# Kernel optimization log

Hardware: AMD Instinct MI355X
Metric: run time of the kernel (lower is better)

Reference implementation:

```python
import jax, jax.numpy as jnp
import numpy as np

N = 50000        # total nodes across batch
K = 16           # max neighbors per node (padded with index 0)
E = 800000       # directed edges / messages
B = 1024         # molecules
MAXM = 48        # max nodes per molecule (padded with index 0)
FEATURE_FDIM = 9
ALL_FDIM = 10    # feature_dist_graph (9) + reshaped rij distance (1)
H = 64           # hidden_dim
NUM_ITERS = 2
NEG_INF = -1e9


def setup_inputs() -> dict:
    key = jax.random.key(0)
    ks = jax.random.split(key, 16)
    s = 1.0 / np.sqrt(H)
    return {
        "target_features": jax.random.normal(ks[0], (N, FEATURE_FDIM), jnp.float32),
        "feature_dist_graph": jax.random.normal(ks[1], (E, ALL_FDIM - 1), jnp.float32),
        "rij_dist_pairs": jax.random.uniform(ks[2], (E,), jnp.float32),
        "start_end_env": jax.random.randint(ks[3], (N, K), 0, N + 1),
        "b_scope": jax.random.randint(ks[4], (N, K), 0, E),
        "l_scope": jax.random.randint(ks[5], (B, MAXM), 0, N + 1),
        "scope_update": jax.random.randint(ks[6], (E,), 0, N + 1),
        "scope_update_lig": jax.random.randint(ks[7], (E,), 0, N + 1),
        "W_emb": jax.random.uniform(ks[8], (FEATURE_FDIM, H), jnp.float32, 0.1, 0.9),
        "b_emb": jnp.zeros((H,), jnp.float32),
        "W_dist": jax.random.uniform(ks[9], (ALL_FDIM, H), jnp.float32, 0.1, 0.9),
        "b_dist": jnp.zeros((H,), jnp.float32),
        "W_gat": jax.random.normal(ks[10], (H, H), jnp.float32) * s,
        "Wm_gat": jax.random.normal(ks[11], (H, H), jnp.float32) * s,
        "a_gat": jax.random.normal(ks[12], (2 * H,), jnp.float32) * s,
    }


def reference(target_features, feature_dist_graph, rij_dist_pairs,
              start_end_env, b_scope, l_scope, scope_update, scope_update_lig,
              W_emb, b_emb, W_dist, b_dist, W_gat, Wm_gat, a_gat):
    # node embedding over origin features
    h = target_features @ W_emb + b_emb                        # [N, H]
    # edge message embedding over pair features + distance
    msg_in = jnp.concatenate([feature_dist_graph, rij_dist_pairs[:, None]], axis=1)
    message = msg_in @ W_dist + b_dist                         # [E, H]
    # prepend zero pad row (index 0 = padding for ragged gathers)
    hp = jnp.concatenate([jnp.zeros((1, H), h.dtype), h], axis=0)  # [N+1, H]
    pad_mask = (start_end_env == 0)                            # [N, K]
    upd_mask = (scope_update_lig > 0).astype(h.dtype)[:, None]  # [E, 1]
    for _ in range(NUM_ITERS):
        nb = hp[start_end_env]                                 # [N, K, H] gather neighbors
        mg = message[b_scope]                                  # [N, K, H] gather messages
        Wn = nb @ W_gat                                        # [N, K, H]
        Wm = mg @ Wm_gat                                       # [N, K, H]
        # GAT attention logits: leaky_relu(a^T [Wn || Wm])
        logits = jax.nn.leaky_relu(
            jnp.einsum('nkh,h->nk', Wn, a_gat[:H]) +
            jnp.einsum('nkh,h->nk', Wm, a_gat[H:]), 0.2)       # [N, K]
        logits = jnp.where(pad_mask, NEG_INF, logits)
        alpha = jax.nn.softmax(logits, axis=1)                 # [N, K]
        new_h = jax.nn.elu(jnp.einsum('nk,nkh->nh', alpha, Wn + Wm))  # [N, H]
        hp = jnp.concatenate([jnp.zeros((1, H), new_h.dtype), new_h], axis=0)
        # scatter updated node features back into edge messages
        message = hp[scope_update] * upd_mask                  # [E, H]
    cmp_enc = hp[l_scope]                                      # [B, MAXM, H]
    return cmp_enc.sum(axis=1)                                 # [B, H]
```

## Files before the change

kernel.cpp:

```cpp
#include <hip/hip_runtime.h>
#include <hip/hip_bf16.h>

#define N_NODES 50000
#define K_NB 16
#define E_EDGES 800000
#define B_MOL 1024
#define MAXM_M 48
#define FDIM 9
#define ADIM 10
#define H 64
#define NEG_INF_F (-1e9f)
#define PRE_NODE_BLOCKS 196
#define EDGE_BLOCKS 3125

typedef __bf16 bf16x8 __attribute__((ext_vector_type(8)));
typedef float f32x4 __attribute__((ext_vector_type(4)));

__device__ inline float readlane_f(float v, int l) {
    return __int_as_float(__builtin_amdgcn_readlane(__float_as_int(v), l));
}
__device__ inline int readlane_i(int v, int l) {
    return __builtin_amdgcn_readlane(v, l);
}
__device__ inline float bf2f(unsigned u) {
    return __uint_as_float(u << 16);
}
__device__ inline unsigned short f2bf(float f) {
    unsigned x = __float_as_uint(f);
    return (unsigned short)((x + 0x7fffu + ((x >> 16) & 1u)) >> 16);
}

#define GLOAD_U16(dst, voff, sbase) \
    asm volatile("global_load_ushort %0, %1, %2" : "=v"(dst) : "v"(voff), "s"(sbase))
#define GLOAD_F32(dst, voff, sbase) \
    asm volatile("global_load_dword %0, %1, %2" : "=v"(dst) : "v"(voff), "s"(sbase))

#define DRAIN16(a) \
    asm volatile("s_waitcnt vmcnt(0)" \
        : "+v"(a[0]), "+v"(a[1]), "+v"(a[2]), "+v"(a[3]), \
          "+v"(a[4]), "+v"(a[5]), "+v"(a[6]), "+v"(a[7]), \
          "+v"(a[8]), "+v"(a[9]), "+v"(a[10]), "+v"(a[11]), \
          "+v"(a[12]), "+v"(a[13]), "+v"(a[14]), "+v"(a[15]))
#define HOLD16(a) \
    asm volatile("" \
        : "+v"(a[0]), "+v"(a[1]), "+v"(a[2]), "+v"(a[3]), \
          "+v"(a[4]), "+v"(a[5]), "+v"(a[6]), "+v"(a[7]), \
          "+v"(a[8]), "+v"(a[9]), "+v"(a[10]), "+v"(a[11]), \
          "+v"(a[12]), "+v"(a[13]), "+v"(a[14]), "+v"(a[15]))

__global__ __launch_bounds__(256) void k_fold(
    const float* __restrict__ W_emb, const float* __restrict__ b_emb,
    const float* __restrict__ W_dist, const float* __restrict__ b_dist,
    const float* __restrict__ W_gat, const float* __restrict__ Wm_gat,
    const float* __restrict__ a_gat,
    float* __restrict__ W2, float* __restrict__ c2,
    float* __restrict__ W3, float* __restrict__ c3,
    float* __restrict__ wa, float* __restrict__ ca,
    float* __restrict__ va, float* __restrict__ vb,
    float* __restrict__ wv9, float* __restrict__ cv,
    unsigned short* __restrict__ WintT)
{
    __shared__ float s_va[64], s_vb[64];
    int tid = threadIdx.x;
    int h = tid & 63, g = tid >> 6;
    if (g == 0) {
        float acc = 0.f;
        for (int t = 0; t < H; ++t) acc += W_gat[h * H + t] * a_gat[t];
        s_va[h] = acc; va[h] = acc;
    } else if (g == 1) {
        float acc = 0.f;
        for (int t = 0; t < H; ++t) acc += Wm_gat[h * H + t] * a_gat[H + t];
        s_vb[h] = acc; vb[h] = acc;
    } else if (g == 2) {
        float acc = 0.f;
        for (int t = 0; t < H; ++t) acc += b_dist[t] * Wm_gat[t * H + h];
        c2[h] = acc;
    } else {
        float acc = 0.f;
        for (int t = 0; t < H; ++t) acc += b_emb[t] * W_gat[t * H + h];
        c3[h] = acc;
    }
    __syncthreads();
    for (int q = tid; q < 640; q += 256) {
        int j = q >> 6, hh = q & 63;
        float acc = 0.f;
        for (int t = 0; t < H; ++t) acc += W_dist[j * H + t] * Wm_gat[t * H + hh];
        W2[q] = acc;
    }
    for (int q = tid; q < 576; q += 256) {
        int j = q >> 6, hh = q & 63;
        float acc = 0.f;
        for (int t = 0; t < H; ++t) acc += W_emb[j * H + t] * W_gat[t * H + hh];
        W3[q] = acc;
    }
    for (int q = tid; q < H * 2 * H; q += 256) {
        int n = q >> 7, k = q & 127;
        float v = (k & 1) ? Wm_gat[(k >> 1) * H + n] : W_gat[(k >> 1) * H + n];
        WintT[q] = f2bf(v);
    }
    if (tid < ADIM) {
        float acc = 0.f;
        for (int t = 0; t < H; ++t) acc += W_dist[tid * H + t] * s_vb[t];
        wa[tid] = acc;
    } else if (tid == ADIM) {
        float acc = 0.f;
        for (int t = 0; t < H; ++t) acc += b_dist[t] * s_vb[t];
        ca[0] = acc;
    } else if (tid >= 16 && tid < 16 + FDIM) {
        int j = tid - 16;
        float acc = 0.f;
        for (int t = 0; t < H; ++t) acc += W_emb[j * H + t] * s_va[t];
        wv9[j] = acc;
    } else if (tid == 31) {
        float acc = 0.f;
        for (int t = 0; t < H; ++t) acc += b_emb[t] * s_va[t];
        cv[0] = acc;
    }
}

__global__ __launch_bounds__(256) void k_pre(
    const float* __restrict__ tf, const float* __restrict__ fdg,
    const float* __restrict__ rij,
    const int* __restrict__ su, const int* __restrict__ sul,
    const float* __restrict__ wa, const float* __restrict__ ca,
    const float* __restrict__ wv9, const float* __restrict__ cv,
    float* __restrict__ t1A, unsigned short* __restrict__ tfp,
    unsigned short* __restrict__ emsg, int* __restrict__ sue)
{
    int bid = blockIdx.x;
    if (bid < PRE_NODE_BLOCKS) {
        int n = bid * 256 + threadIdx.x;
        if (n == 0) {
            t1A[0] = 0.f;
            uint4 z = make_uint4(0, 0, 0, 0);
            ((uint4*)tfp)[0] = z; ((uint4*)tfp)[1] = z;
        }
        if (n >= N_NODES) return;
        float f[FDIM];
        float acc = cv[0];
#pragma unroll
        for (int j = 0; j < FDIM; ++j) {
            f[j] = tf[n * FDIM + j];
            acc += f[j] * wv9[j];
        }
        t1A[n + 1] = acc;
        unsigned rec[8];
#pragma unroll
        for (int j = 0; j < 4; ++j)
            rec[j] = (unsigned)f2bf(f[2 * j]) | ((unsigned)f2bf(f[2 * j + 1]) << 16);
        rec[4] = (unsigned)f2bf(f[8]);
        rec[5] = 0; rec[6] = 0; rec[7] = 0;
        uint4* dst = (uint4*)(tfp + (size_t)(n + 1) * 16);
        dst[0] = make_uint4(rec[0], rec[1], rec[2], rec[3]);
        dst[1] = make_uint4(rec[4], rec[5], rec[6], rec[7]);
    } else {
        int e = (bid - PRE_NODE_BLOCKS) * 256 + threadIdx.x;
        float f[ADIM];
#pragma unroll
        for (int j = 0; j < FDIM; ++j) f[j] = fdg[(size_t)e * FDIM + j];
        f[FDIM] = rij[e];
        float acc = ca[0];
#pragma unroll
        for (int j = 0; j < ADIM; ++j) acc += f[j] * wa[j];
        unsigned rec[8];
#pragma unroll
        for (int j = 0; j < 5; ++j)
            rec[j] = (unsigned)f2bf(f[2 * j]) | ((unsigned)f2bf(f[2 * j + 1]) << 16);
        rec[5] = __float_as_uint(acc);
        rec[6] = 0; rec[7] = 0;
        uint4* dst = (uint4*)(emsg + (size_t)e * 16);
        dst[0] = make_uint4(rec[0], rec[1], rec[2], rec[3]);
        dst[1] = make_uint4(rec[4], rec[5], rec[6], rec[7]);
        sue[e] = (sul[e] > 0) ? su[e] : 0;
    }
}

__global__ __launch_bounds__(256) void k_gat1(
    const int* __restrict__ sse, const int* __restrict__ bsc,
    const float* __restrict__ t1A, const unsigned short* __restrict__ tfp,
    const unsigned short* __restrict__ emsg,
    const float* __restrict__ W2, const float* __restrict__ c2,
    const float* __restrict__ W3, const float* __restrict__ c3,
    const float* __restrict__ va, const float* __restrict__ vb,
    unsigned short* __restrict__ hp2bf, float* __restrict__ t1B,
    float* __restrict__ t2B)
{
    int wave = threadIdx.x >> 6;
    int lane = threadIdx.x & 63;
    int n = blockIdx.x * 4 + wave;
    if (n == 0) {
        hp2bf[lane] = 0;
        if (lane == 0) { t1B[0] = 0.f; t2B[0] = 0.f; }
    }
    if (n >= N_NODES) return;

    int kidx = 0, ke = 0;
    float lg = NEG_INF_F;
    if (lane < K_NB) {
        kidx = sse[n * K_NB + lane];
        ke   = bsc[n * K_NB + lane];
        float g2 = __uint_as_float(*(const unsigned*)(emsg + (size_t)ke * 16 + 10));
        float p = t1A[kidx] + g2;
        p = (p > 0.f) ? p : 0.2f * p;
        lg = (kidx == 0) ? NEG_INF_F : p;
    }

    unsigned wn_u[K_NB], wm_u[K_NB];
    int offr = (lane & 15) * 2;
#pragma unroll
    for (int k = 0; k < K_NB; ++k) {
        const unsigned short* pk = tfp + (size_t)readlane_i(kidx, k) * 16;
        GLOAD_U16(wn_u[k], offr, pk);
    }
#pragma unroll
    for (int k = 0; k < K_NB; ++k) {
        const unsigned short* pe = emsg + (size_t)readlane_i(ke, k) * 16;
        GLOAD_U16(wm_u[k], offr, pe);
    }

    float m = lg;
#pragma unroll
    for (int o = 8; o > 0; o >>= 1) m = fmaxf(m, __shfl_xor(m, o, 64));
    float ex = __expf(lg - m);
    float s = ex;
#pragma unroll
    for (int o = 8; o > 0; o >>= 1) s += __shfl_xor(s, o, 64);
    float alpha = ex / s;

    DRAIN16(wn_u);
    HOLD16(wm_u);

    float fr = 0.f, frm = 0.f, beta = 0.f;
#pragma unroll
    for (int k = 0; k < K_NB; ++k) {
        float ak = readlane_f(alpha, k);
        fr  += ak * bf2f(wn_u[k]);
        frm += ak * bf2f(wm_u[k]);
        beta += (readlane_i(kidx, k) > 0) ? ak : 0.f;
    }
    float acc = c2[lane] + beta * c3[lane];
#pragma unroll
    for (int j = 0; j < FDIM; ++j) acc += readlane_f(fr, j) * W3[j * H + lane];
#pragma unroll
    for (int j = 0; j < ADIM; ++j) acc += readlane_f(frm, j) * W2[j * H + lane];
    float o = (acc > 0.f) ? acc : expm1f(acc);
    hp2bf[(size_t)(n + 1) * H + lane] = f2bf(o);
    float ta = o * va[lane], tb = o * vb[lane];
#pragma unroll
    for (int q = 32; q > 0; q >>= 1) {
        ta += __shfl_xor(ta, q, 64);
        tb += __shfl_xor(tb, q, 64);
    }
    if (lane == 0) { t1B[n + 1] = ta; t2B[n + 1] = tb; }
}

__global__ __launch_bounds__(1024) void k_gat2(
    const int* __restrict__ sse, const int* __restrict__ bsc,
    const int* __restrict__ sue,
    const float* __restrict__ t1B, const float* __restrict__ t2B,
    const unsigned short* __restrict__ hp2bf,
    const unsigned short* __restrict__ WintT,
    float* __restrict__ hp3)
{
    __shared__ unsigned s_rows[16][72];
    int wave = threadIdx.x >> 6;
    int lane = threadIdx.x & 63;
    int row  = blockIdx.x * 16 + wave;
    int n    = row - 1;

    float gn = 0.f, gm = 0.f;
    if (n >= 0 && n < N_NODES) {
        int kidx = 0, ksu = 0;
        float lg = NEG_INF_F;
        if (lane < K_NB) {
            kidx = sse[n * K_NB + lane];
            int ke = bsc[n * K_NB + lane];
            ksu = sue[ke];
            float p = t1B[kidx] + t2B[ksu];
            p = (p > 0.f) ? p : 0.2f * p;
            lg = (kidx == 0) ? NEG_INF_F : p;
        }

        unsigned wn_u[K_NB], wm_u[K_NB];
        int off = lane * 2;
#pragma unroll
        for (int k = 0; k < K_NB; ++k) {
            const unsigned short* pk = hp2bf + (size_t)readlane_i(kidx, k) * H;
            GLOAD_U16(wn_u[k], off, pk);
        }
#pragma unroll
        for (int k = 0; k < K_NB; ++k) {
            const unsigned short* ps = hp2bf + (size_t)readlane_i(ksu, k) * H;
            GLOAD_U16(wm_u[k], off, ps);
        }

        float m = lg;
#pragma unroll
        for (int o = 8; o > 0; o >>= 1) m = fmaxf(m, __shfl_xor(m, o, 64));
        float ex = __expf(lg - m);
        float s = ex;
#pragma unroll
        for (int o = 8; o > 0; o >>= 1) s += __shfl_xor(s, o, 64);
        float alpha = ex / s;

        DRAIN16(wn_u);
        HOLD16(wm_u);

#pragma unroll
        for (int k = 0; k < K_NB; ++k) {
            float ak = readlane_f(alpha, k);
            gn += ak * bf2f(wn_u[k]);
            gm += ak * bf2f(wm_u[k]);
        }
    }
    s_rows[wave][lane] = (unsigned)f2bf(gn) | ((unsigned)f2bf(gm) << 16);
    __syncthreads();

    if (wave < 4) {
        int t = wave;
        int m = lane & 15, q = lane >> 4;
        union UB { uint4 u; bf16x8 v; };
        bf16x8 bfr[4];
        const unsigned short* bp = WintT + (size_t)(t * 16 + m) * 128 + q * 8;
#pragma unroll
        for (int kk = 0; kk < 4; ++kk) {
            UB ub; ub.u = *(const uint4*)(bp + kk * 32);
            bfr[kk] = ub.v;
        }
        f32x4 acc = (f32x4){0.f, 0.f, 0.f, 0.f};
#pragma unroll
        for (int kk = 0; kk < 4; ++kk) {
            UB ua; ua.u = *(const uint4*)&s_rows[m][kk * 16 + q * 4];
            acc = __builtin_amdgcn_mfma_f32_16x16x32_bf16(ua.v, bfr[kk], acc, 0, 0, 0);
        }
        int row0 = blockIdx.x * 16;
#pragma unroll
        for (int r = 0; r < 4; ++r) {
            int rr = row0 + q * 4 + r;
            if (rr <= N_NODES) {
                float v = acc[r];
                hp3[(size_t)rr * H + t * 16 + m] = (v > 0.f) ? v : expm1f(v);
            }
        }
    }
}

__global__ __launch_bounds__(256) void k_out(
    const int* __restrict__ l_scope, const float* __restrict__ hp,
    float* __restrict__ out)
{
    int wave = threadIdx.x >> 6;
    int lane = threadIdx.x & 63;
    int b = blockIdx.x * 4 + wave;
    if (b >= B_MOL) return;
    int idx48 = (lane < MAXM_M) ? l_scope[b * MAXM_M + lane] : 0;
    float v[MAXM_M];
    int off = lane * 4;
#pragma unroll
    for (int m = 0; m < MAXM_M; ++m) {
        const float* pm = hp + (size_t)readlane_i(idx48, m) * H;
        GLOAD_F32(v[m], off, pm);
    }
    asm volatile("s_waitcnt vmcnt(0)"
        : "+v"(v[0]), "+v"(v[1]), "+v"(v[2]), "+v"(v[3]),
          "+v"(v[4]), "+v"(v[5]), "+v"(v[6]), "+v"(v[7]),
          "+v"(v[8]), "+v"(v[9]), "+v"(v[10]), "+v"(v[11]),
          "+v"(v[12]), "+v"(v[13]), "+v"(v[14]), "+v"(v[15]));
    asm volatile(""
        : "+v"(v[16]), "+v"(v[17]), "+v"(v[18]), "+v"(v[19]),
          "+v"(v[20]), "+v"(v[21]), "+v"(v[22]), "+v"(v[23]),
          "+v"(v[24]), "+v"(v[25]), "+v"(v[26]), "+v"(v[27]),
          "+v"(v[28]), "+v"(v[29]), "+v"(v[30]), "+v"(v[31]));
    asm volatile(""
        : "+v"(v[32]), "+v"(v[33]), "+v"(v[34]), "+v"(v[35]),
          "+v"(v[36]), "+v"(v[37]), "+v"(v[38]), "+v"(v[39]),
          "+v"(v[40]), "+v"(v[41]), "+v"(v[42]), "+v"(v[43]),
          "+v"(v[44]), "+v"(v[45]), "+v"(v[46]), "+v"(v[47]));
    float acc = 0.f;
#pragma unroll
    for (int m = 0; m < MAXM_M; ++m) acc += v[m];
    out[b * H + lane] = acc;
}

extern "C" void kernel_launch(void* const* d_in, const int* in_sizes, int n_in,
                              void* d_out, int out_size, void* d_ws, size_t ws_size,
                              hipStream_t stream)
{
    const float* tf     = (const float*)d_in[0];
    const float* fdg    = (const float*)d_in[1];
    const float* rij    = (const float*)d_in[2];
    const int*   sse    = (const int*)d_in[3];
    const int*   bsc    = (const int*)d_in[4];
    const int*   lsc    = (const int*)d_in[5];
    const int*   su     = (const int*)d_in[6];
    const int*   sul    = (const int*)d_in[7];
    const float* W_emb  = (const float*)d_in[8];
    const float* b_emb  = (const float*)d_in[9];
    const float* W_dist = (const float*)d_in[10];
    const float* b_dist = (const float*)d_in[11];
    const float* W_gat  = (const float*)d_in[12];
    const float* Wm_gat = (const float*)d_in[13];
    const float* a_gat  = (const float*)d_in[14];
    float* out = (float*)d_out;

    char* base = (char*)d_ws;
    size_t off = 0;
    auto alloc = [&](size_t bytes) {
        char* p = base + off;
        off = (off + bytes + 255) & ~(size_t)255;
        return p;
    };
    float* W2   = (float*)alloc(640 * 4);
    float* c2   = (float*)alloc(64 * 4);
    float* W3   = (float*)alloc(640 * 4);
    float* c3   = (float*)alloc(64 * 4);
    float* wa   = (float*)alloc(16 * 4);
    float* ca   = (float*)alloc(16 * 4);
    float* va   = (float*)alloc(64 * 4);
    float* vb   = (float*)alloc(64 * 4);
    float* wv9  = (float*)alloc(16 * 4);
    float* cv   = (float*)alloc(16 * 4);
    unsigned short* WintT = (unsigned short*)alloc(64 * 128 * 2);
    float* t1A  = (float*)alloc((size_t)(N_NODES + 1) * 4);
    float* t1B  = (float*)alloc((size_t)(N_NODES + 1) * 4);
    float* t2B  = (float*)alloc((size_t)(N_NODES + 1) * 4);
    int*   sue  = (int*)alloc((size_t)E_EDGES * 4);
    unsigned short* tfp   = (unsigned short*)alloc((size_t)(N_NODES + 1) * 16 * 2);
    unsigned short* hp2bf = (unsigned short*)alloc((size_t)(N_NODES + 1) * H * 2);
    char* big = alloc((size_t)E_EDGES * 32);
    unsigned short* emsg = (unsigned short*)big;
    float* hp3 = (float*)big;

    k_fold<<<dim3(1), dim3(256), 0, stream>>>(
        W_emb, b_emb, W_dist, b_dist, W_gat, Wm_gat, a_gat,
        W2, c2, W3, c3, wa, ca, va, vb, wv9, cv, WintT);

    k_pre<<<dim3(PRE_NODE_BLOCKS + EDGE_BLOCKS), dim3(256), 0, stream>>>(
        tf, fdg, rij, su, sul, wa, ca, wv9, cv, t1A, tfp, emsg, sue);

    k_gat1<<<dim3((N_NODES + 3) / 4), dim3(256), 0, stream>>>(
        sse, bsc, t1A, tfp, emsg, W2, c2, W3, c3, va, vb, hp2bf, t1B, t2B);

    k_gat2<<<dim3((N_NODES + 16) / 16), dim3(1024), 0, stream>>>(
        sse, bsc, sue, t1B, t2B, hp2bf, WintT, hp3);

    k_out<<<dim3(B_MOL / 4), dim3(256), 0, stream>>>(lsc, hp3, out);
}
```

Measured before the change: 209.1 us.

## Gather neighbor rows with 16-byte loads and reduce across lanes in k_gat2

Replaces the 32 per-lane 2-byte gathers per node with four dwordx4 loads per lane. Each group of 8 lanes fetches one full 128-byte neighbor row, and the alpha-weighted partial sums are then reduced across row groups with xor shuffles. The feature-row loads are issued before the attention logit and softmax computation so that the memory latency overlaps with it. This cuts the number of memory instructions, at the cost of 48 extra cross-lane shuffles for the reduction. It also adds a launch-bounds occupancy hint, which may force register limits.

```diff
diff --git a/kernel.cpp b/kernel.cpp
--- a/kernel.cpp
+++ b/kernel.cpp
@@ -15,6 +15,7 @@
 
 typedef __bf16 bf16x8 __attribute__((ext_vector_type(8)));
 typedef float f32x4 __attribute__((ext_vector_type(4)));
+typedef unsigned u32x4 __attribute__((ext_vector_type(4)));
 
 __device__ inline float readlane_f(float v, int l) {
     return __int_as_float(__builtin_amdgcn_readlane(__float_as_int(v), l));
@@ -34,6 +35,8 @@
     asm volatile("global_load_ushort %0, %1, %2" : "=v"(dst) : "v"(voff), "s"(sbase))
 #define GLOAD_F32(dst, voff, sbase) \
     asm volatile("global_load_dword %0, %1, %2" : "=v"(dst) : "v"(voff), "s"(sbase))
+#define GLOAD_X4(dst, addr) \
+    asm volatile("global_load_dwordx4 %0, %1, off" : "=v"(dst) : "v"(addr))
 
 #define DRAIN16(a) \
     asm volatile("s_waitcnt vmcnt(0)" \
@@ -47,6 +50,8 @@
           "+v"(a[4]), "+v"(a[5]), "+v"(a[6]), "+v"(a[7]), \
           "+v"(a[8]), "+v"(a[9]), "+v"(a[10]), "+v"(a[11]), \
           "+v"(a[12]), "+v"(a[13]), "+v"(a[14]), "+v"(a[15]))
+#define DRAIN4X4(a, b, c, d) \
+    asm volatile("s_waitcnt vmcnt(0)" : "+v"(a), "+v"(b), "+v"(c), "+v"(d))
 
 __global__ __launch_bounds__(256) void k_fold(
     const float* __restrict__ W_emb, const float* __restrict__ b_emb,
@@ -254,7 +259,7 @@
     if (lane == 0) { t1B[n + 1] = ta; t2B[n + 1] = tb; }
 }
 
-__global__ __launch_bounds__(1024) void k_gat2(
+__global__ __launch_bounds__(1024, 8) void k_gat2(
     const int* __restrict__ sse, const int* __restrict__ bsc,
     const int* __restrict__ sue,
     const float* __restrict__ t1B, const float* __restrict__ t2B,
@@ -268,7 +273,10 @@
     int row  = blockIdx.x * 16 + wave;
     int n    = row - 1;
 
-    float gn = 0.f, gm = 0.f;
+    float accn[8], accm[8];
+#pragma unroll
+    for (int q = 0; q < 8; ++q) { accn[q] = 0.f; accm[q] = 0.f; }
+
     if (n >= 0 && n < N_NODES) {
         int kidx = 0, ksu = 0;
         float lg = NEG_INF_F;
@@ -276,24 +284,30 @@
             kidx = sse[n * K_NB + lane];
             int ke = bsc[n * K_NB + lane];
             ksu = sue[ke];
-            float p = t1B[kidx] + t2B[ksu];
-            p = (p > 0.f) ? p : 0.2f * p;
-            lg = (kidx == 0) ? NEG_INF_F : p;
-        }
-
-        unsigned wn_u[K_NB], wm_u[K_NB];
-        int off = lane * 2;
-#pragma unroll
-        for (int k = 0; k < K_NB; ++k) {
-            const unsigned short* pk = hp2bf + (size_t)readlane_i(kidx, k) * H;
-            GLOAD_U16(wn_u[k], off, pk);
-        }
-#pragma unroll
-        for (int k = 0; k < K_NB; ++k) {
-            const unsigned short* ps = hp2bf + (size_t)readlane_i(ksu, k) * H;
-            GLOAD_U16(wm_u[k], off, ps);
-        }
-
+        }
+
+        int r = lane >> 3;
+        int p = lane & 7;
+        int kn0 = __shfl(kidx, r, 64);
+        int kn1 = __shfl(kidx, r + 8, 64);
+        int km0 = __shfl(ksu,  r, 64);
+        int km1 = __shfl(ksu,  r + 8, 64);
+
+        u32x4 vn0, vn1, vm0, vm1;
+        const uint4* a0 = (const uint4*)(hp2bf + (size_t)kn0 * H) + p;
+        const uint4* a1 = (const uint4*)(hp2bf + (size_t)kn1 * H) + p;
+        const uint4* a2 = (const uint4*)(hp2bf + (size_t)km0 * H) + p;
+        const uint4* a3 = (const uint4*)(hp2bf + (size_t)km1 * H) + p;
+        GLOAD_X4(vn0, a0);
+        GLOAD_X4(vn1, a1);
+        GLOAD_X4(vm0, a2);
+        GLOAD_X4(vm1, a3);
+
+        if (lane < K_NB) {
+            float pg = t1B[kidx] + t2B[ksu];
+            pg = (pg > 0.f) ? pg : 0.2f * pg;
+            lg = (kidx == 0) ? NEG_INF_F : pg;
+        }
         float m = lg;
 #pragma unroll
         for (int o = 8; o > 0; o >>= 1) m = fmaxf(m, __shfl_xor(m, o, 64));
@@ -303,17 +317,38 @@
         for (int o = 8; o > 0; o >>= 1) s += __shfl_xor(s, o, 64);
         float alpha = ex / s;
 
-        DRAIN16(wn_u);
-        HOLD16(wm_u);
-
-#pragma unroll
-        for (int k = 0; k < K_NB; ++k) {
-            float ak = readlane_f(alpha, k);
-            gn += ak * bf2f(wn_u[k]);
-            gm += ak * bf2f(wm_u[k]);
-        }
-    }
-    s_rows[wave][lane] = (unsigned)f2bf(gn) | ((unsigned)f2bf(gm) << 16);
+        float a_r0 = __shfl(alpha, r, 64);
+        float a_r1 = __shfl(alpha, r + 8, 64);
+
+        DRAIN4X4(vn0, vn1, vm0, vm1);
+
+#pragma unroll
+        for (int q = 0; q < 4; ++q) {
+            unsigned w0 = vn0[q], w1 = vn1[q], w2 = vm0[q], w3 = vm1[q];
+            accn[2 * q]     += a_r0 * bf2f(w0 & 0xffffu) + a_r1 * bf2f(w1 & 0xffffu);
+            accn[2 * q + 1] += a_r0 * bf2f(w0 >> 16)     + a_r1 * bf2f(w1 >> 16);
+            accm[2 * q]     += a_r0 * bf2f(w2 & 0xffffu) + a_r1 * bf2f(w3 & 0xffffu);
+            accm[2 * q + 1] += a_r0 * bf2f(w2 >> 16)     + a_r1 * bf2f(w3 >> 16);
+        }
+#pragma unroll
+        for (int o = 8; o <= 32; o <<= 1) {
+#pragma unroll
+            for (int q = 0; q < 8; ++q) {
+                accn[q] += __shfl_xor(accn[q], o, 64);
+                accm[q] += __shfl_xor(accm[q], o, 64);
+            }
+        }
+    }
+
+    if (lane < 8) {
+        unsigned outp[8];
+#pragma unroll
+        for (int q = 0; q < 8; ++q)
+            outp[q] = (unsigned)f2bf(accn[q]) | ((unsigned)f2bf(accm[q]) << 16);
+        uint4* d = (uint4*)&s_rows[wave][lane * 8];
+        d[0] = make_uint4(outp[0], outp[1], outp[2], outp[3]);
+        d[1] = make_uint4(outp[4], outp[5], outp[6], outp[7]);
+    }
     __syncthreads();
 
     if (wave < 4) {
```

New measurement: 216.0 us. 3.3% more time.

## Split gat2 gathers into two row-range phases and precompose ksu index lookup

Applied to the files above, without the earlier changes.

k_gat2 now runs twice as many blocks, each phase gathering only neighbor/message rows within half of the node range, so each phase's working set of hp2bf is smaller and more cache-resident. Each phase writes a partial pre-activation into an interleaved buffer, and k_out sums the two partials and applies ELU. A new k_ksu kernel precomposes su/sul through b_scope into a per-(n,k) index array, removing a dependent indirect load from gat2. The cost is doubled attention/softmax/MFMA work in gat2, an extra kernel launch, twice the hp3 write traffic, and extra branching in the gather loops.

```diff
diff --git a/kernel.cpp b/kernel.cpp
--- a/kernel.cpp
+++ b/kernel.cpp
@@ -12,9 +12,12 @@
 #define NEG_INF_F (-1e9f)
 #define PRE_NODE_BLOCKS 196
 #define EDGE_BLOCKS 3125
+#define GAT2_NB 3126
+#define ROW_SPLIT 25000
 
 typedef __bf16 bf16x8 __attribute__((ext_vector_type(8)));
 typedef float f32x4 __attribute__((ext_vector_type(4)));
+typedef float f32x2 __attribute__((ext_vector_type(2)));
 
 __device__ inline float readlane_f(float v, int l) {
     return __int_as_float(__builtin_amdgcn_readlane(__float_as_int(v), l));
@@ -32,8 +35,8 @@
 
 #define GLOAD_U16(dst, voff, sbase) \
     asm volatile("global_load_ushort %0, %1, %2" : "=v"(dst) : "v"(voff), "s"(sbase))
-#define GLOAD_F32(dst, voff, sbase) \
-    asm volatile("global_load_dword %0, %1, %2" : "=v"(dst) : "v"(voff), "s"(sbase))
+#define GLOAD_F32X2(dst, voff, sbase) \
+    asm volatile("global_load_dwordx2 %0, %1, %2" : "=v"(dst) : "v"(voff), "s"(sbase))
 
 #define DRAIN16(a) \
     asm volatile("s_waitcnt vmcnt(0)" \
@@ -47,6 +50,12 @@
           "+v"(a[4]), "+v"(a[5]), "+v"(a[6]), "+v"(a[7]), \
           "+v"(a[8]), "+v"(a[9]), "+v"(a[10]), "+v"(a[11]), \
           "+v"(a[12]), "+v"(a[13]), "+v"(a[14]), "+v"(a[15]))
+#define HOLD16R(a, base) \
+    asm volatile("" \
+        : "+v"(a[base + 0]), "+v"(a[base + 1]), "+v"(a[base + 2]), "+v"(a[base + 3]), \
+          "+v"(a[base + 4]), "+v"(a[base + 5]), "+v"(a[base + 6]), "+v"(a[base + 7]), \
+          "+v"(a[base + 8]), "+v"(a[base + 9]), "+v"(a[base + 10]), "+v"(a[base + 11]), \
+          "+v"(a[base + 12]), "+v"(a[base + 13]), "+v"(a[base + 14]), "+v"(a[base + 15]))
 
 __global__ __launch_bounds__(256) void k_fold(
     const float* __restrict__ W_emb, const float* __restrict__ b_emb,
@@ -121,11 +130,10 @@
 __global__ __launch_bounds__(256) void k_pre(
     const float* __restrict__ tf, const float* __restrict__ fdg,
     const float* __restrict__ rij,
-    const int* __restrict__ su, const int* __restrict__ sul,
     const float* __restrict__ wa, const float* __restrict__ ca,
     const float* __restrict__ wv9, const float* __restrict__ cv,
     float* __restrict__ t1A, unsigned short* __restrict__ tfp,
-    unsigned short* __restrict__ emsg, int* __restrict__ sue)
+    unsigned short* __restrict__ emsg)
 {
     int bid = blockIdx.x;
     if (bid < PRE_NODE_BLOCKS) {
@@ -171,8 +179,16 @@
         uint4* dst = (uint4*)(emsg + (size_t)e * 16);
         dst[0] = make_uint4(rec[0], rec[1], rec[2], rec[3]);
         dst[1] = make_uint4(rec[4], rec[5], rec[6], rec[7]);
-        sue[e] = (sul[e] > 0) ? su[e] : 0;
-    }
+    }
+}
+
+__global__ __launch_bounds__(256) void k_ksu(
+    const int* __restrict__ bsc, const int* __restrict__ su,
+    const int* __restrict__ sul, int* __restrict__ ksu_nk)
+{
+    int i = blockIdx.x * 256 + threadIdx.x;
+    int e = bsc[i];
+    ksu_nk[i] = (sul[e] > 0) ? su[e] : 0;
 }
 
 __global__ __launch_bounds__(256) void k_gat1(
@@ -255,17 +271,21 @@
 }
 
 __global__ __launch_bounds__(1024) void k_gat2(
-    const int* __restrict__ sse, const int* __restrict__ bsc,
-    const int* __restrict__ sue,
+    const int* __restrict__ sse, const int* __restrict__ ksu_nk,
     const float* __restrict__ t1B, const float* __restrict__ t2B,
     const unsigned short* __restrict__ hp2bf,
     const unsigned short* __restrict__ WintT,
-    float* __restrict__ hp3)
+    float* __restrict__ hp3pp)
 {
     __shared__ unsigned s_rows[16][72];
+    int bid  = blockIdx.x;
+    int phase = (bid >= GAT2_NB) ? 1 : 0;
+    int nb   = bid - phase * GAT2_NB;
+    int lo   = phase ? ROW_SPLIT : 0;
+    int hi   = phase ? (N_NODES + 1) : ROW_SPLIT;
     int wave = threadIdx.x >> 6;
     int lane = threadIdx.x & 63;
-    int row  = blockIdx.x * 16 + wave;
+    int row  = nb * 16 + wave;
     int n    = row - 1;
 
     float gn = 0.f, gm = 0.f;
@@ -274,8 +294,7 @@
         float lg = NEG_INF_F;
         if (lane < K_NB) {
             kidx = sse[n * K_NB + lane];
-            int ke = bsc[n * K_NB + lane];
-            ksu = sue[ke];
+            ksu  = ksu_nk[n * K_NB + lane];
             float p = t1B[kidx] + t2B[ksu];
             p = (p > 0.f) ? p : 0.2f * p;
             lg = (kidx == 0) ? NEG_INF_F : p;
@@ -285,13 +304,21 @@
         int off = lane * 2;
 #pragma unroll
         for (int k = 0; k < K_NB; ++k) {
-            const unsigned short* pk = hp2bf + (size_t)readlane_i(kidx, k) * H;
-            GLOAD_U16(wn_u[k], off, pk);
+            wn_u[k] = 0u;
+            int rk = readlane_i(kidx, k);
+            if (rk >= lo && rk < hi) {
+                const unsigned short* pk = hp2bf + (size_t)rk * H;
+                GLOAD_U16(wn_u[k], off, pk);
+            }
         }
 #pragma unroll
         for (int k = 0; k < K_NB; ++k) {
-            const unsigned short* ps = hp2bf + (size_t)readlane_i(ksu, k) * H;
-            GLOAD_U16(wm_u[k], off, ps);
+            wm_u[k] = 0u;
+            int rs = readlane_i(ksu, k);
+            if (rs >= lo && rs < hi) {
+                const unsigned short* ps = hp2bf + (size_t)rs * H;
+                GLOAD_U16(wm_u[k], off, ps);
+            }
         }
 
         float m = lg;
@@ -333,20 +360,18 @@
             UB ua; ua.u = *(const uint4*)&s_rows[m][kk * 16 + q * 4];
             acc = __builtin_amdgcn_mfma_f32_16x16x32_bf16(ua.v, bfr[kk], acc, 0, 0, 0);
         }
-        int row0 = blockIdx.x * 16;
+        int row0 = nb * 16;
 #pragma unroll
         for (int r = 0; r < 4; ++r) {
             int rr = row0 + q * 4 + r;
-            if (rr <= N_NODES) {
-                float v = acc[r];
-                hp3[(size_t)rr * H + t * 16 + m] = (v > 0.f) ? v : expm1f(v);
-            }
+            if (rr >= 1 && rr <= N_NODES)
+                hp3pp[((size_t)(rr - 1) * H + t * 16 + m) * 2 + phase] = acc[r];
         }
     }
 }
 
 __global__ __launch_bounds__(256) void k_out(
-    const int* __restrict__ l_scope, const float* __restrict__ hp,
+    const int* __restrict__ l_scope, const float* __restrict__ hp3pp,
     float* __restrict__ out)
 {
     int wave = threadIdx.x >> 6;
@@ -354,12 +379,16 @@
     int b = blockIdx.x * 4 + wave;
     if (b >= B_MOL) return;
     int idx48 = (lane < MAXM_M) ? l_scope[b * MAXM_M + lane] : 0;
-    float v[MAXM_M];
-    int off = lane * 4;
+    f32x2 v[MAXM_M];
+    int off = lane * 8;
 #pragma unroll
     for (int m = 0; m < MAXM_M; ++m) {
-        const float* pm = hp + (size_t)readlane_i(idx48, m) * H;
-        GLOAD_F32(v[m], off, pm);
+        v[m] = (f32x2){0.f, 0.f};
+        int idx = readlane_i(idx48, m);
+        if (idx > 0) {
+            const float* pm = hp3pp + (size_t)(idx - 1) * (H * 2);
+            GLOAD_F32X2(v[m], off, pm);
+        }
     }
     asm volatile("s_waitcnt vmcnt(0)"
         : "+v"(v[0]), "+v"(v[1]), "+v"(v[2]), "+v"(v[3]),
@@ -378,7 +407,10 @@
           "+v"(v[44]), "+v"(v[45]), "+v"(v[46]), "+v"(v[47]));
     float acc = 0.f;
 #pragma unroll
-    for (int m = 0; m < MAXM_M; ++m) acc += v[m];
+    for (int m = 0; m < MAXM_M; ++m) {
+        float w = v[m][0] + v[m][1];
+        acc += (w > 0.f) ? w : expm1f(w);
+    }
     out[b * H + lane] = acc;
 }
 
@@ -424,25 +456,27 @@
     float* t1A  = (float*)alloc((size_t)(N_NODES + 1) * 4);
     float* t1B  = (float*)alloc((size_t)(N_NODES + 1) * 4);
     float* t2B  = (float*)alloc((size_t)(N_NODES + 1) * 4);
-    int*   sue  = (int*)alloc((size_t)E_EDGES * 4);
+    int*   ksu_nk = (int*)alloc((size_t)E_EDGES * 4);
     unsigned short* tfp   = (unsigned short*)alloc((size_t)(N_NODES + 1) * 16 * 2);
     unsigned short* hp2bf = (unsigned short*)alloc((size_t)(N_NODES + 1) * H * 2);
     char* big = alloc((size_t)E_EDGES * 32);
     unsigned short* emsg = (unsigned short*)big;
-    float* hp3 = (float*)big;
+    float* hp3pp = (float*)big;
 
     k_fold<<<dim3(1), dim3(256), 0, stream>>>(
         W_emb, b_emb, W_dist, b_dist, W_gat, Wm_gat, a_gat,
         W2, c2, W3, c3, wa, ca, va, vb, wv9, cv, WintT);
 
     k_pre<<<dim3(PRE_NODE_BLOCKS + EDGE_BLOCKS), dim3(256), 0, stream>>>(
-        tf, fdg, rij, su, sul, wa, ca, wv9, cv, t1A, tfp, emsg, sue);
+        tf, fdg, rij, wa, ca, wv9, cv, t1A, tfp, emsg);
+
+    k_ksu<<<dim3(EDGE_BLOCKS), dim3(256), 0, stream>>>(bsc, su, sul, ksu_nk);
 
     k_gat1<<<dim3((N_NODES + 3) / 4), dim3(256), 0, stream>>>(
         sse, bsc, t1A, tfp, emsg, W2, c2, W3, c3, va, vb, hp2bf, t1B, t2B);
 
-    k_gat2<<<dim3((N_NODES + 16) / 16), dim3(1024), 0, stream>>>(
-        sse, bsc, sue, t1B, t2B, hp2bf, WintT, hp3);
-
-    k_out<<<dim3(B_MOL / 4), dim3(256), 0, stream>>>(lsc, hp3, out);
-}
+    k_gat2<<<dim3(2 * GAT2_NB), dim3(1024), 0, stream>>>(
+        sse, ksu_nk, t1B, t2B, hp2bf, WintT, hp3pp);
+
+    k_out<<<dim3(B_MOL / 4), dim3(256), 0, stream>>>(lsc, hp3pp, out);
+}
```

After: 259.6 us. 1.24x slower.
